# Optimization experiments

Hardware: AMD Instinct MI355X
Metric: run time of the kernel (lower is better)

## Reference

```python
import jax, jax.numpy as jnp
import numpy as np

D_MODEL = 2048
NUM_HEADS = 16
HEAD_DIM = D_MODEL // NUM_HEADS
B, T = 2, 2048


def setup_inputs() -> dict:
    key = jax.random.key(0)
    ks = jax.random.split(key, 6)
    x = jax.random.normal(ks[0], (B, T, D_MODEL), dtype=jnp.float32)
    # RoPE tables: angles theta_i = 10000^(-2i/d), half-dim tables [T, HEAD_DIM//2]
    pos = jnp.arange(T, dtype=jnp.float32)[:, None]
    inv_freq = 1.0 / (10000.0 ** (jnp.arange(0, HEAD_DIM, 2, dtype=jnp.float32) / HEAD_DIM))
    ang = pos * inv_freq[None, :]
    sin = jnp.sin(ang)
    cos = jnp.cos(ang)
    doc_ids = jnp.sort(jax.random.randint(ks[1], (B, T), 0, 4), axis=-1).astype(jnp.int32)
    W_qkv = jax.random.normal(ks[2], (D_MODEL, D_MODEL + 2 * HEAD_DIM), dtype=jnp.float32) * 0.02
    W_out = jax.random.normal(ks[3], (D_MODEL, D_MODEL), dtype=jnp.float32) * 0.02
    return {"x": x, "sin": sin, "cos": cos, "doc_ids": doc_ids, "W_qkv": W_qkv, "W_out": W_out}


def _apply_rope(x, sin, cos):
    # x: [..., T, ..., HEAD_DIM]; sin/cos: [T, HEAD_DIM//2], broadcast to x's rank
    if x.ndim == 4:  # [B, T, H, D]
        s, c = sin[None, :, None, :], cos[None, :, None, :]
    else:  # [B, T, D]
        s, c = sin[None, :, :], cos[None, :, :]
    x1, x2 = jnp.split(x, 2, axis=-1)
    return jnp.concatenate([x1 * c - x2 * s, x2 * c + x1 * s], axis=-1)


def reference(x, sin, cos, doc_ids, W_qkv, W_out):
    b, t, _ = x.shape
    qkv = x @ W_qkv  # [B, T, D_MODEL + 2*HEAD_DIM]
    q = qkv[..., :D_MODEL].reshape(b, t, NUM_HEADS, HEAD_DIM)
    k = qkv[..., D_MODEL:D_MODEL + HEAD_DIM]  # [B, T, HEAD_DIM] single KV head
    v = qkv[..., D_MODEL + HEAD_DIM:]         # [B, T, HEAD_DIM]
    q = _apply_rope(q, sin, cos)
    k = _apply_rope(k, sin, cos)
    # doc-packed causal mask -> additive bias [B, 1, T, T]
    neg_inf = jnp.finfo(q.dtype).min / 2
    causal = jnp.tril(jnp.ones((t, t), dtype=jnp.bool_))
    same_doc = doc_ids[:, :, None] == doc_ids[:, None, :]
    mask = (causal[None, :, :] & same_doc)[:, None, :, :]
    bias = jnp.where(mask, jnp.array(0.0, q.dtype), neg_inf)
    scale = 1.0 / jnp.sqrt(jnp.array(HEAD_DIM, q.dtype))
    scores = jnp.einsum("bthd,bsd->bhts", q, k) * scale + bias  # [B, H, T, T]
    attn = jax.nn.softmax(scores, axis=-1)
    out = jnp.einsum("bhts,bsd->bthd", attn, v).reshape(b, t, D_MODEL)
    return out @ W_out
```

## Files before the change

kernel.cpp:

```cpp
#include <hip/hip_runtime.h>
#include <math.h>

#define D_MODEL 2048
#define NUM_HEADS 16
#define HEAD_DIM 128
#define BB 2
#define TT 2048
#define QKV_N 2304
#define KOFF 2048
#define VOFF 2176

typedef __attribute__((ext_vector_type(8))) short short8;
typedef __attribute__((ext_vector_type(4))) float f32x4;

static __device__ __forceinline__ short f2bf(float f) {
  union { float f; unsigned u; } x; x.f = f;
  unsigned r = (x.u + 0x7FFFu + ((x.u >> 16) & 1u)) >> 16;
  return (short)r;
}

#define GLD16(gp, lp)                                              \
  __builtin_amdgcn_global_load_lds(                                \
      (const __attribute__((address_space(1))) void*)(gp),         \
      (__attribute__((address_space(3))) void*)(lp), 16, 0, 0)

static __device__ __forceinline__ void swizzle_xy(int& bx, int& by) {
  const int gx = gridDim.x;
  const int lin = blockIdx.y * gx + blockIdx.x;
  const int band = lin / (gx * 8);
  const int rem = lin - band * gx * 8;
  by = band * 8 + (rem & 7);
  bx = rem >> 3;
}

__global__ __launch_bounds__(256) void gemm_qkv_rope(
    const short* __restrict__ A, const short* __restrict__ Bt,
    short* __restrict__ qkv, short* __restrict__ Vtb,
    const float* __restrict__ sin_t, const float* __restrict__ cos_t)
{
  __shared__ short As[2 * 128 * 32];
  __shared__ short Bs[2 * 128 * 32];
  const int K = D_MODEL;

  int bx, by;
  swizzle_xy(bx, by);

  const int tid = threadIdx.x;
  const int w = tid >> 6, l = tid & 63;
  const int quad = l >> 4, l16 = l & 15;
  const int wm = w >> 1, wn = w & 1;
  const int m0 = by * 128, n0 = bx * 128;

  f32x4 acc[4][4];
#pragma unroll
  for (int i = 0; i < 4; i++)
#pragma unroll
    for (int j = 0; j < 4; j++) acc[i][j] = (f32x4){0.f, 0.f, 0.f, 0.f};

  const int cswz = ((l & 3) ^ ((l >> 3) & 3)) * 8;
  const short* aA = A + (size_t)(m0 + w * 32 + (l >> 2)) * K + cswz;
  const short* aB = Bt + (size_t)(n0 + w * 32 + (l >> 2)) * K + cswz;
  short* lA = As + w * 1024;
  short* lB = Bs + w * 1024;

  const int aswz = (quad ^ ((l16 >> 1) & 3)) * 8;
  const short* Ard = As + (size_t)(wm * 64 + l16) * 32 + aswz;
  const short* Brd = Bs + (size_t)(wn * 16 + l16) * 32 + aswz;

  for (int k0 = 0; k0 < K; k0 += 64) {
    __syncthreads();
#pragma unroll
    for (int h = 0; h < 2; h++) {
      const int go = k0 + h * 32;
      const int lo = h * 4096;
      GLD16(aA + go, lA + lo);
      GLD16(aA + go + (size_t)16 * K, lA + lo + 512);
      GLD16(aB + go, lB + lo);
      GLD16(aB + go + (size_t)16 * K, lB + lo + 512);
    }
    __syncthreads();

#pragma unroll
    for (int kc = 0; kc < 2; kc++) {
      short8 af[4], bf[4];
#pragma unroll
      for (int mi = 0; mi < 4; mi++)
        af[mi] = *(const short8*)(Ard + kc * 4096 + mi * 512);
#pragma unroll
      for (int ni = 0; ni < 4; ni++)
        bf[ni] = *(const short8*)(Brd + kc * 4096 + ni * 1024);
#pragma unroll
      for (int mi = 0; mi < 4; mi++)
#pragma unroll
        for (int ni = 0; ni < 4; ni++)
          acc[mi][ni] =
              __builtin_amdgcn_mfma_f32_16x16x32_bf16(af[mi], bf[ni], acc[mi][ni], 0, 0, 0);
    }
  }

  const int colbase = wn * 16 + l16;
  const bool is_v = (n0 == VOFF);

#pragma unroll
  for (int mi = 0; mi < 4; mi++) {
#pragma unroll
    for (int r = 0; r < 4; r++) {
      const int row = m0 + wm * 64 + mi * 16 + quad * 4 + r;
      const int b = row >> 11, t = row & (TT - 1);
#pragma unroll
      for (int ni = 0; ni < 2; ni++) {
        const int cloc = ni * 32 + colbase;
        const float c1 = acc[mi][ni][r];
        const float c2 = acc[mi][ni + 2][r];
        if (!is_v) {
          const float sn = sin_t[t * 64 + cloc];
          const float cs = cos_t[t * 64 + cloc];
          short* op = qkv + (size_t)row * QKV_N + n0 + cloc;
          op[0]  = f2bf(c1 * cs - c2 * sn);
          op[64] = f2bf(c2 * cs + c1 * sn);
        } else {
          Vtb[((size_t)(b * 128 + cloc) << 11) + t]      = f2bf(c1);
          Vtb[((size_t)(b * 128 + cloc + 64) << 11) + t] = f2bf(c2);
        }
      }
    }
  }
}

__global__ __launch_bounds__(256) void gemm_mfma_bt(
    const short* __restrict__ A, const short* __restrict__ Bt,
    float* __restrict__ C, int M, int N, int K)
{
  __shared__ short As[2 * 128 * 32];
  __shared__ short Bs[2 * 128 * 32];

  int bx, by;
  swizzle_xy(bx, by);

  const int tid = threadIdx.x;
  const int w = tid >> 6, l = tid & 63;
  const int quad = l >> 4, l16 = l & 15;
  const int wm = w >> 1, wn = w & 1;
  const int m0 = by * 128, n0 = bx * 128;

  f32x4 acc[4][4];
#pragma unroll
  for (int i = 0; i < 4; i++)
#pragma unroll
    for (int j = 0; j < 4; j++) acc[i][j] = (f32x4){0.f, 0.f, 0.f, 0.f};

  const int cswz = ((l & 3) ^ ((l >> 3) & 3)) * 8;
  const short* aA = A + (size_t)(m0 + w * 32 + (l >> 2)) * K + cswz;
  const short* aB = Bt + (size_t)(n0 + w * 32 + (l >> 2)) * K + cswz;
  short* lA = As + w * 1024;
  short* lB = Bs + w * 1024;

  const int aswz = (quad ^ ((l16 >> 1) & 3)) * 8;
  const short* Ard = As + (size_t)(wm * 64 + l16) * 32 + aswz;
  const short* Brd = Bs + (size_t)(wn * 64 + l16) * 32 + aswz;

  for (int k0 = 0; k0 < K; k0 += 64) {
    __syncthreads();
#pragma unroll
    for (int h = 0; h < 2; h++) {
      const int go = k0 + h * 32;
      const int lo = h * 4096;
      GLD16(aA + go, lA + lo);
      GLD16(aA + go + (size_t)16 * K, lA + lo + 512);
      GLD16(aB + go, lB + lo);
      GLD16(aB + go + (size_t)16 * K, lB + lo + 512);
    }
    __syncthreads();

#pragma unroll
    for (int kc = 0; kc < 2; kc++) {
      short8 af[4], bf[4];
#pragma unroll
      for (int mi = 0; mi < 4; mi++)
        af[mi] = *(const short8*)(Ard + kc * 4096 + mi * 512);
#pragma unroll
      for (int ni = 0; ni < 4; ni++)
        bf[ni] = *(const short8*)(Brd + kc * 4096 + ni * 512);
#pragma unroll
      for (int mi = 0; mi < 4; mi++)
#pragma unroll
        for (int ni = 0; ni < 4; ni++)
          acc[mi][ni] =
              __builtin_amdgcn_mfma_f32_16x16x32_bf16(af[mi], bf[ni], acc[mi][ni], 0, 0, 0);
    }
  }

#pragma unroll
  for (int mi = 0; mi < 4; mi++) {
#pragma unroll
    for (int ni = 0; ni < 4; ni++) {
#pragma unroll
      for (int r = 0; r < 4; r++) {
        const int row = m0 + wm * 64 + mi * 16 + quad * 4 + r;
        const int col = n0 + wn * 64 + ni * 16 + l16;
        C[(size_t)row * N + col] = acc[mi][ni][r];
      }
    }
  }
}

#define XB_BLOCKS 8192
#define WQ_BLOCKS (72 * 64)
#define WO_BLOCKS (64 * 64)

__global__ __launch_bounds__(256) void prep_all(
    const float* __restrict__ x, short* __restrict__ xb,
    const float* __restrict__ Wq, short* __restrict__ Wqt,
    const float* __restrict__ Wo, short* __restrict__ Wot)
{
  const int bid = blockIdx.x;
  const int tid = threadIdx.x;

  if (bid < XB_BLOCKS) {
    const size_t i4 = (size_t)bid * 256 + tid;
    float4 v = *(const float4*)(x + i4 * 4);
    short4 o;
    o.x = f2bf(v.x); o.y = f2bf(v.y); o.z = f2bf(v.z); o.w = f2bf(v.w);
    *(short4*)(xb + i4 * 4) = o;
    return;
  }

  __shared__ float t[32][33];
  const float* W;
  short* Wt;
  int N, tile, ntx;
  if (bid < XB_BLOCKS + WQ_BLOCKS) {
    tile = bid - XB_BLOCKS; W = Wq; Wt = Wqt; N = QKV_N; ntx = 72;
  } else {
    tile = bid - XB_BLOCKS - WQ_BLOCKS; W = Wo; Wt = Wot; N = D_MODEL; ntx = 64;
  }
  const int K = D_MODEL;
  const int bx = tile % ntx, byy = tile / ntx;
  const int tx = tid & 31, ty = tid >> 5;
  const int n0 = bx * 32, k0 = byy * 32;
#pragma unroll
  for (int j = 0; j < 4; j++)
    t[ty + j * 8][tx] = W[(size_t)(k0 + ty + j * 8) * N + n0 + tx];
  __syncthreads();
#pragma unroll
  for (int j = 0; j < 4; j++)
    Wt[(size_t)(n0 + ty + j * 8) * K + k0 + tx] = f2bf(t[tx][ty + j * 8]);
}

#define PSTR 72

__global__ __launch_bounds__(256, 2) void attn_mfma(
    const short* __restrict__ qkv, const short* __restrict__ Vtb,
    const int* __restrict__ doc_ids, short* __restrict__ attn_out)
{
  __shared__ short Ks[64 * 128];
  __shared__ short Vt[128 * 64];
  __shared__ short Pbuf[4 * 16 * PSTR];
  __shared__ int doc_s[64];

  const int qt = blockIdx.x, h0 = blockIdx.y * 2, b = blockIdx.z;
  const int q0 = qt * 64;
  const int tid = threadIdx.x;
  const int w = tid >> 6;
  const int lane = tid & 63;
  const int quad = lane >> 4, l16 = lane & 15;

  short8 Qf[2][4];
#pragma unroll
  for (int hh = 0; hh < 2; hh++) {
    const short* qp = qkv + (size_t)(b * TT + q0 + w * 16 + l16) * QKV_N
                      + (h0 + hh) * HEAD_DIM + quad * 8;
#pragma unroll
    for (int kc = 0; kc < 4; kc++) Qf[hh][kc] = *(const short8*)(qp + kc * 32);
  }

  const int docmin_q = doc_ids[b * TT + q0];
  const int docmax_q = doc_ids[b * TT + q0 + 63];

  int qg[4], mydoc[4];
#pragma unroll
  for (int r = 0; r < 4; r++) {
    qg[r] = q0 + w * 16 + quad * 4 + r;
    mydoc[r] = doc_ids[b * TT + qg[r]];
  }
  float l_i[2][4];
  f32x4 O[2][8];
#pragma unroll
  for (int hh = 0; hh < 2; hh++) {
#pragma unroll
    for (int r = 0; r < 4; r++) l_i[hh][r] = 0.f;
#pragma unroll
    for (int v8 = 0; v8 < 8; v8++) O[hh][v8] = (f32x4){0.f, 0.f, 0.f, 0.f};
  }

  short* Pw = Pbuf + w * 16 * PSTR;
  const float scale = 0.08838834764831844f;

  const int x7 = l16 & 7;
  int kcol[4], vcol[2];
#pragma unroll
  for (int kc = 0; kc < 4; kc++) kcol[kc] = ((kc * 4 + quad) ^ x7) * 8;
#pragma unroll
  for (int ks = 0; ks < 2; ks++) vcol[ks] = ((ks * 4 + quad) ^ x7) * 8;

  for (int st = 0; st <= qt; st++) {
    const int s0 = st * 64;
    const int dmin_s = doc_ids[b * TT + s0];
    const int dmax_s = doc_ids[b * TT + s0 + 63];
    if (dmax_s < docmin_q) continue;
    const bool full = (st < qt) && (dmin_s == docmax_q);

    __syncthreads();
#pragma unroll
    for (int j = 0; j < 4; j++) {
      const int f = w * 4 + j;
      const int rg = f * 4 + (lane >> 4);
      GLD16(qkv + (size_t)(b * TT + s0 + rg) * QKV_N + KOFF
                + (((lane & 15) ^ (rg & 7)) * 8),
            Ks + f * 512);
    }
#pragma unroll
    for (int j = 0; j < 4; j++) {
      const int f = w * 4 + j;
      const int n = f * 8 + (lane >> 3);
      GLD16(Vtb + (((size_t)(b * 128 + n)) << 11) + s0
                + (((lane & 7) ^ (lane >> 3)) * 8),
            Vt + f * 512);
    }
    if (!full && tid < 64) doc_s[tid] = doc_ids[b * TT + s0 + tid];
    __syncthreads();

#pragma unroll
    for (int hh = 0; hh < 2; hh++) {
      f32x4 S[4];
#pragma unroll
      for (int ns = 0; ns < 4; ns++) {
        f32x4 acc = (f32x4){0.f, 0.f, 0.f, 0.f};
        const short* krow = Ks + (ns * 16 + l16) * 128;
#pragma unroll
        for (int kc = 0; kc < 4; kc++) {
          short8 kf = *(const short8*)(krow + kcol[kc]);
          acc = __builtin_amdgcn_mfma_f32_16x16x32_bf16(Qf[hh][kc], kf, acc, 0, 0, 0);
        }
        S[ns] = acc;
      }

      if (full) {
#pragma unroll
        for (int ns = 0; ns < 4; ns++)
#pragma unroll
          for (int r = 0; r < 4; r++) {
            const float p = __expf(S[ns][r] * scale);
            l_i[hh][r] += p;
            Pw[(quad * 4 + r) * PSTR + ns * 16 + l16] = f2bf(p);
          }
      } else {
#pragma unroll
        for (int ns = 0; ns < 4; ns++) {
          const int s_loc = ns * 16 + l16;
          const int sg = s0 + s_loc;
          const int sdoc = doc_s[s_loc];
#pragma unroll
          for (int r = 0; r < 4; r++) {
            const bool ok = (sg <= qg[r]) && (sdoc == mydoc[r]);
            const float p = ok ? __expf(S[ns][r] * scale) : 0.f;
            l_i[hh][r] += p;
            Pw[(quad * 4 + r) * PSTR + ns * 16 + l16] = f2bf(p);
          }
        }
      }

#pragma unroll
      for (int ks = 0; ks < 2; ks++) {
        short8 pf = *(const short8*)(Pw + l16 * PSTR + ks * 32 + quad * 8);
#pragma unroll
        for (int v8 = 0; v8 < 8; v8++) {
          short8 vf = *(const short8*)(Vt + (v8 * 16 + l16) * 64 + vcol[ks]);
          O[hh][v8] = __builtin_amdgcn_mfma_f32_16x16x32_bf16(pf, vf, O[hh][v8], 0, 0, 0);
        }
      }
    }
  }

#pragma unroll
  for (int hh = 0; hh < 2; hh++) {
#pragma unroll
    for (int off = 8; off >= 1; off >>= 1)
#pragma unroll
      for (int r = 0; r < 4; r++) l_i[hh][r] += __shfl_xor(l_i[hh][r], off);

#pragma unroll
    for (int r = 0; r < 4; r++) {
      const float inv = 1.f / l_i[hh][r];
      short* op = attn_out + (size_t)(b * TT + qg[r]) * D_MODEL
                  + (h0 + hh) * HEAD_DIM + l16;
#pragma unroll
      for (int v8 = 0; v8 < 8; v8++)
        op[v8 * 16] = f2bf(O[hh][v8][r] * inv);
    }
  }
}

extern "C" void kernel_launch(void* const* d_in, const int* in_sizes, int n_in,
                              void* d_out, int out_size, void* d_ws, size_t ws_size,
                              hipStream_t stream)
{
  const float* x     = (const float*)d_in[0];
  const float* sin_t = (const float*)d_in[1];
  const float* cos_t = (const float*)d_in[2];
  const int*   doc   = (const int*)  d_in[3];
  const float* W_qkv = (const float*)d_in[4];
  const float* W_out = (const float*)d_in[5];
  float* out = (float*)d_out;

  const int M = BB * TT;

  char* p = (char*)d_ws;
  short* qkv_bf = (short*)p; p += (size_t)M * QKV_N * 2;
  short* xb     = (short*)p; p += (size_t)M * D_MODEL * 2;
  short* attn_bf = xb;
  short* Vtb    = (short*)p; p += (size_t)BB * 128 * TT * 2;
  short* Wqkv_t = (short*)p; p += (size_t)QKV_N * D_MODEL * 2;
  short* Wout_t = (short*)p;

  prep_all<<<XB_BLOCKS + WQ_BLOCKS + WO_BLOCKS, 256, 0, stream>>>(
      x, xb, W_qkv, Wqkv_t, W_out, Wout_t);

  {
    dim3 grid(QKV_N / 128, M / 128);
    gemm_qkv_rope<<<grid, 256, 0, stream>>>(xb, Wqkv_t, qkv_bf, Vtb, sin_t, cos_t);
  }
  {
    dim3 grid(TT / 64, NUM_HEADS / 2, BB);
    attn_mfma<<<grid, 256, 0, stream>>>(qkv_bf, Vtb, doc, attn_bf);
  }
  {
    dim3 grid(D_MODEL / 128, M / 128);
    gemm_mfma_bt<<<grid, 256, 0, stream>>>(attn_bf, Wout_t, out, M, D_MODEL, D_MODEL);
  }
}
```

Measured before the change: 273.4 us.

## Pair mirrored query tiles per attention block to balance causal work

Each attention block now handles one head and two query tiles (qt and 31-qt) instead of one query tile for two heads. Each loaded K/V tile is shared by both query tiles, and every block gets a similar amount of causal work, so the tail of long-running blocks shrinks. In exchange, K/V reuse across two heads is lost. The per-tile active, full and doc checks become more complex, and the grid now has 16x16x2 blocks.

```diff
diff --git a/kernel.cpp b/kernel.cpp
--- a/kernel.cpp
+++ b/kernel.cpp
@@ -258,39 +258,37 @@
   __shared__ short Pbuf[4 * 16 * PSTR];
   __shared__ int doc_s[64];
 
-  const int qt = blockIdx.x, h0 = blockIdx.y * 2, b = blockIdx.z;
-  const int q0 = qt * 64;
+  const int h = blockIdx.y, b = blockIdx.z;
+  const int qt0 = blockIdx.x;
+  const int qt1 = 31 - qt0;
   const int tid = threadIdx.x;
   const int w = tid >> 6;
   const int lane = tid & 63;
   const int quad = lane >> 4, l16 = lane & 15;
 
   short8 Qf[2][4];
-#pragma unroll
-  for (int hh = 0; hh < 2; hh++) {
-    const short* qp = qkv + (size_t)(b * TT + q0 + w * 16 + l16) * QKV_N
-                      + (h0 + hh) * HEAD_DIM + quad * 8;
-#pragma unroll
-    for (int kc = 0; kc < 4; kc++) Qf[hh][kc] = *(const short8*)(qp + kc * 32);
-  }
-
-  const int docmin_q = doc_ids[b * TT + q0];
-  const int docmax_q = doc_ids[b * TT + q0 + 63];
-
-  int qg[4], mydoc[4];
-#pragma unroll
-  for (int r = 0; r < 4; r++) {
-    qg[r] = q0 + w * 16 + quad * 4 + r;
-    mydoc[r] = doc_ids[b * TT + qg[r]];
-  }
+  int qg[2][4], mydoc[2][4];
   float l_i[2][4];
   f32x4 O[2][8];
-#pragma unroll
-  for (int hh = 0; hh < 2; hh++) {
-#pragma unroll
-    for (int r = 0; r < 4; r++) l_i[hh][r] = 0.f;
-#pragma unroll
-    for (int v8 = 0; v8 < 8; v8++) O[hh][v8] = (f32x4){0.f, 0.f, 0.f, 0.f};
+  int docmin[2], docmax[2];
+
+#pragma unroll
+  for (int qi = 0; qi < 2; qi++) {
+    const int q0 = (qi ? qt1 : qt0) * 64;
+    const short* qp = qkv + (size_t)(b * TT + q0 + w * 16 + l16) * QKV_N
+                      + h * HEAD_DIM + quad * 8;
+#pragma unroll
+    for (int kc = 0; kc < 4; kc++) Qf[qi][kc] = *(const short8*)(qp + kc * 32);
+    docmin[qi] = doc_ids[b * TT + q0];
+    docmax[qi] = doc_ids[b * TT + q0 + 63];
+#pragma unroll
+    for (int r = 0; r < 4; r++) {
+      qg[qi][r] = q0 + w * 16 + quad * 4 + r;
+      mydoc[qi][r] = doc_ids[b * TT + qg[qi][r]];
+      l_i[qi][r] = 0.f;
+    }
+#pragma unroll
+    for (int v8 = 0; v8 < 8; v8++) O[qi][v8] = (f32x4){0.f, 0.f, 0.f, 0.f};
   }
 
   short* Pw = Pbuf + w * 16 * PSTR;
@@ -303,12 +301,16 @@
 #pragma unroll
   for (int ks = 0; ks < 2; ks++) vcol[ks] = ((ks * 4 + quad) ^ x7) * 8;
 
-  for (int st = 0; st <= qt; st++) {
+  for (int st = 0; st <= qt1; st++) {
     const int s0 = st * 64;
     const int dmin_s = doc_ids[b * TT + s0];
     const int dmax_s = doc_ids[b * TT + s0 + 63];
-    if (dmax_s < docmin_q) continue;
-    const bool full = (st < qt) && (dmin_s == docmax_q);
+    const bool act0 = (st <= qt0) && (dmax_s >= docmin[0]);
+    const bool act1 = (dmax_s >= docmin[1]);
+    if (!act0 && !act1) continue;
+    const bool full0 = (st < qt0) && (dmin_s == docmax[0]);
+    const bool full1 = (st < qt1) && (dmin_s == docmax[1]);
+    const bool needdoc = (act0 && !full0) || (act1 && !full1);
 
     __syncthreads();
 #pragma unroll
@@ -327,11 +329,15 @@
                 + (((lane & 7) ^ (lane >> 3)) * 8),
             Vt + f * 512);
     }
-    if (!full && tid < 64) doc_s[tid] = doc_ids[b * TT + s0 + tid];
-    __syncthreads();
-
-#pragma unroll
-    for (int hh = 0; hh < 2; hh++) {
+    if (needdoc && tid < 64) doc_s[tid] = doc_ids[b * TT + s0 + tid];
+    __syncthreads();
+
+#pragma unroll
+    for (int qi = 0; qi < 2; qi++) {
+      const bool act = qi ? act1 : act0;
+      if (!act) continue;
+      const bool full = qi ? full1 : full0;
+
       f32x4 S[4];
 #pragma unroll
       for (int ns = 0; ns < 4; ns++) {
@@ -340,7 +346,7 @@
 #pragma unroll
         for (int kc = 0; kc < 4; kc++) {
           short8 kf = *(const short8*)(krow + kcol[kc]);
-          acc = __builtin_amdgcn_mfma_f32_16x16x32_bf16(Qf[hh][kc], kf, acc, 0, 0, 0);
+          acc = __builtin_amdgcn_mfma_f32_16x16x32_bf16(Qf[qi][kc], kf, acc, 0, 0, 0);
         }
         S[ns] = acc;
       }
@@ -351,7 +357,7 @@
 #pragma unroll
           for (int r = 0; r < 4; r++) {
             const float p = __expf(S[ns][r] * scale);
-            l_i[hh][r] += p;
+            l_i[qi][r] += p;
             Pw[(quad * 4 + r) * PSTR + ns * 16 + l16] = f2bf(p);
           }
       } else {
@@ -362,9 +368,9 @@
           const int sdoc = doc_s[s_loc];
 #pragma unroll
           for (int r = 0; r < 4; r++) {
-            const bool ok = (sg <= qg[r]) && (sdoc == mydoc[r]);
+            const bool ok = (sg <= qg[qi][r]) && (sdoc == mydoc[qi][r]);
             const float p = ok ? __expf(S[ns][r] * scale) : 0.f;
-            l_i[hh][r] += p;
+            l_i[qi][r] += p;
             Pw[(quad * 4 + r) * PSTR + ns * 16 + l16] = f2bf(p);
           }
         }
@@ -376,27 +382,27 @@
 #pragma unroll
         for (int v8 = 0; v8 < 8; v8++) {
           short8 vf = *(const short8*)(Vt + (v8 * 16 + l16) * 64 + vcol[ks]);
-          O[hh][v8] = __builtin_amdgcn_mfma_f32_16x16x32_bf16(pf, vf, O[hh][v8], 0, 0, 0);
+          O[qi][v8] = __builtin_amdgcn_mfma_f32_16x16x32_bf16(pf, vf, O[qi][v8], 0, 0, 0);
         }
       }
     }
   }
 
 #pragma unroll
-  for (int hh = 0; hh < 2; hh++) {
+  for (int qi = 0; qi < 2; qi++) {
 #pragma unroll
     for (int off = 8; off >= 1; off >>= 1)
 #pragma unroll
-      for (int r = 0; r < 4; r++) l_i[hh][r] += __shfl_xor(l_i[hh][r], off);
+      for (int r = 0; r < 4; r++) l_i[qi][r] += __shfl_xor(l_i[qi][r], off);
 
 #pragma unroll
     for (int r = 0; r < 4; r++) {
-      const float inv = 1.f / l_i[hh][r];
-      short* op = attn_out + (size_t)(b * TT + qg[r]) * D_MODEL
-                  + (h0 + hh) * HEAD_DIM + l16;
+      const float inv = 1.f / l_i[qi][r];
+      short* op = attn_out + (size_t)(b * TT + qg[qi][r]) * D_MODEL
+                  + h * HEAD_DIM + l16;
 #pragma unroll
       for (int v8 = 0; v8 < 8; v8++)
-        op[v8 * 16] = f2bf(O[hh][v8][r] * inv);
+        op[v8 * 16] = f2bf(O[qi][v8][r] * inv);
     }
   }
 }
@@ -431,7 +437,7 @@
     gemm_qkv_rope<<<grid, 256, 0, stream>>>(xb, Wqkv_t, qkv_bf, Vtb, sin_t, cos_t);
   }
   {
-    dim3 grid(TT / 64, NUM_HEADS / 2, BB);
+    dim3 grid(TT / 128, NUM_HEADS, BB);
     attn_mfma<<<grid, 256, 0, stream>>>(qkv_bf, Vtb, doc, attn_bf);
   }
   {
```

Result: faster. 258.9 us (-5.3%).
